# Kernel tuning notes

Hardware: AMD Instinct MI355X
Metric: run time of the kernel (lower is better)

## Reference

```python
import jax, jax.numpy as jnp
import numpy as np

B, S, H = 2, 512, 768
E, M, R, R2 = 64, 64, 128, 128
NER_C, REL_C, SIZE_E, CLS = 10, 8, 32, 101
NEG = -1e30


def _linear(x, w, b):
    # torch nn.Linear convention: w is [out, in]
    return x @ w.T + b


def _span_pool(emb, masks):
    # emb [B,S,H], masks [B,K,S] -> masked max over tokens -> [B,K,H]
    neg = jnp.where(masks[..., None] != 0, 0.0, NEG)  # [B,K,S,1]
    return jnp.max(neg + emb[:, None, :, :], axis=2)


def _classify_spans(input_ids, emb, masks, size_emb, rep_w, rep_b, head_w, head_b):
    pool = _span_pool(emb, masks)                      # [B,K,H]
    cls_idx = jnp.argmax((input_ids == CLS).astype(jnp.int32), axis=1)
    ctx = emb[jnp.arange(emb.shape[0]), cls_idx]       # [B,H] (get_token)
    rep = jnp.concatenate([jnp.broadcast_to(ctx[:, None, :], pool.shape), pool, size_emb], axis=-1)
    clf = _linear(jax.nn.relu(_linear(rep, rep_w, rep_b)), head_w, head_b)
    return clf, pool


def _classify_relations(pool, size_emb, rels, rel_masks, emb, w1, b1, w2, b2, w3, b3):
    Bc = pool.shape[0]
    bidx = jnp.arange(Bc)[:, None, None]
    pairs = pool[bidx, rels].reshape(Bc, rels.shape[1], -1)        # [B,R,2H]
    size_pairs = size_emb[bidx, rels].reshape(Bc, rels.shape[1], -1)  # [B,R,2*SIZE_E]
    # masked max over context tokens (rel mask)
    ctx = jnp.max(jnp.where(rel_masks[..., None] != 0, 0.0, NEG) + emb[:, None, :, :], axis=2)
    ctx = jnp.where(jnp.any(rel_masks != 0, axis=-1)[..., None], ctx, 0.0)
    rel_repr = jnp.concatenate([ctx, pairs, size_pairs], axis=-1)  # [B,R,3H+2*SIZE_E]
    h = jax.nn.relu(_linear(rel_repr, w1, b1))
    h = jax.nn.relu(_linear(h, w2, b2))
    return _linear(h, w3, b3)


def setup_inputs():
    key = jax.random.key(0)
    ks = jax.random.split(key, 24)
    p = lambda k, shape: jax.random.normal(k, shape, jnp.float32) * 0.02
    ids = jax.random.randint(ks[0], (B, S), 2000, 30000)
    ids = ids.at[:, 0].set(CLS)  # exactly one cls token per row
    return dict(
        input_ids=ids,
        entity_masks=jax.random.randint(ks[1], (B, E, S), 0, 2).astype(jnp.int32),
        entity_sizes=jax.random.randint(ks[2], (B, E), 0, 100),
        mention_masks=jax.random.randint(ks[3], (B, M, S), 0, 2).astype(jnp.int32),
        mention_sizes=jax.random.randint(ks[4], (B, M), 0, 100),
        relations=jax.random.randint(ks[5], (B, R, 2), 0, E),
        rel_masks=jax.random.randint(ks[6], (B, R, S), 0, 2).astype(jnp.int32),
        references=jax.random.randint(ks[7], (B, R2, 2), 0, M),
        references_masks=jax.random.randint(ks[8], (B, R2, S), 0, 2).astype(jnp.int32),
        token_embedding=jax.random.normal(ks[9], (B, S, H), jnp.float32),
        ner_size_emb=p(ks[10], (100, SIZE_E)),
        emd_size_emb=p(ks[11], (100, SIZE_E)),
        ner_rep_w=p(ks[12], (H, 2 * H + SIZE_E)), ner_rep_b=jnp.zeros(H, jnp.float32),
        ner_head_w=p(ks[13], (NER_C, H)), ner_head_b=jnp.zeros(NER_C, jnp.float32),
        emd_rep_w=p(ks[14], (H, 2 * H + SIZE_E)), emd_rep_b=jnp.zeros(H, jnp.float32),
        emd_head_w=p(ks[15], (2, H)), emd_head_b=jnp.zeros(2, jnp.float32),
        rel_w1=p(ks[16], (H, 3 * H + 2 * SIZE_E)), rel_b1=jnp.zeros(H, jnp.float32),
        rel_w2=p(ks[17], (H, H)), rel_b2=jnp.zeros(H, jnp.float32),
        rel_w3=p(ks[18], (REL_C, H)), rel_b3=jnp.zeros(REL_C, jnp.float32),
        cr_w1=p(ks[19], (H, 3 * H + 2 * SIZE_E)), cr_b1=jnp.zeros(H, jnp.float32),
        cr_w2=p(ks[20], (H, H)), cr_b2=jnp.zeros(H, jnp.float32),
        cr_w3=p(ks[21], (1, H)), cr_b3=jnp.zeros(1, jnp.float32),
    )


def reference(input_ids, entity_masks, entity_sizes, mention_masks, mention_sizes,
              relations, rel_masks, references, references_masks, token_embedding,
              ner_size_emb, emd_size_emb,
              ner_rep_w, ner_rep_b, ner_head_w, ner_head_b,
              emd_rep_w, emd_rep_b, emd_head_w, emd_head_b,
              rel_w1, rel_b1, rel_w2, rel_b2, rel_w3, rel_b3,
              cr_w1, cr_b1, cr_w2, cr_b2, cr_w3, cr_b3):
    sz = ner_size_emb[entity_sizes]                                    # [B,E,SIZE_E]
    entity_clf, entity_pool = _classify_spans(input_ids, token_embedding, entity_masks, sz,
                                              ner_rep_w, ner_rep_b, ner_head_w, ner_head_b)
    rel_clf = _classify_relations(entity_pool, sz, relations, rel_masks, token_embedding,
                                  rel_w1, rel_b1, rel_w2, rel_b2, rel_w3, rel_b3)
    msz = emd_size_emb[mention_sizes]
    mention_clf, mention_pool = _classify_spans(input_ids, token_embedding, mention_masks, msz,
                                                emd_rep_w, emd_rep_b, emd_head_w, emd_head_b)
    ref_clf = _classify_relations(mention_pool, msz, references, references_masks, token_embedding,
                                  cr_w1, cr_b1, cr_w2, cr_b2, cr_w3, cr_b3)
    return entity_clf, rel_clf, mention_clf, ref_clf
```

## Files before the change

### kernel.cpp

```cpp
#include <hip/hip_runtime.h>
#include <hip/hip_bf16.h>

typedef __hip_bfloat16 bf16;
typedef __attribute__((ext_vector_type(8))) short short8;
typedef __attribute__((ext_vector_type(4))) float f32x4;

#define SS 512
#define HD 768
#define NEGC (-1e30f)

#define WOFF_NER 0
#define WOFF_EMD 1204224
#define WOFF_RW1 2408448
#define WOFF_CW1 4227072
#define WOFF_RW2 6045696
#define WOFF_CW2 6635520
#define W_TOT    7225344
#define CVT_BLOCKS (W_TOT / 4 / 256)

__global__ __launch_bounds__(256) void k_pool_cvt(
    const int* __restrict__ e_masks, const int* __restrict__ m_masks,
    const int* __restrict__ r_masks, const int* __restrict__ c_masks,
    const float* __restrict__ emb, bf16* __restrict__ part, int* __restrict__ flags,
    const float* __restrict__ s0, const float* __restrict__ s1,
    const float* __restrict__ s2, const float* __restrict__ s3,
    const float* __restrict__ s4, const float* __restrict__ s5,
    bf16* __restrict__ wdst)
{
  int bx = blockIdx.x;
  int t  = threadIdx.x;

  if (bx >= 768) {
    size_t i = ((size_t)(bx - 768) * 256 + t) * 4;
    const float* s; size_t off;
    if      (i < WOFF_EMD) { s = s0; off = i; }
    else if (i < WOFF_RW1) { s = s1; off = i - WOFF_EMD; }
    else if (i < WOFF_CW1) { s = s2; off = i - WOFF_RW1; }
    else if (i < WOFF_RW2) { s = s3; off = i - WOFF_CW1; }
    else if (i < WOFF_CW2) { s = s4; off = i - WOFF_RW2; }
    else                   { s = s5; off = i - WOFF_CW2; }
    float4 v = *(const float4*)(s + off);
    wdst[i]     = __hip_bfloat16(v.x);
    wdst[i + 1] = __hip_bfloat16(v.y);
    wdst[i + 2] = __hip_bfloat16(v.z);
    wdst[i + 3] = __hip_bfloat16(v.w);
    return;
  }

  int g  = bx % 48;
  int b  = (bx / 48) & 1;
  int sp = bx / 96;
  int j0 = g * 8;

  const int* marr; int row0;
  if      (j0 < 64)  { marr = e_masks; row0 = b*64  +  j0;        }
  else if (j0 < 128) { marr = m_masks; row0 = b*64  + (j0-64);    }
  else if (j0 < 256) { marr = r_masks; row0 = b*128 + (j0-128);   }
  else               { marr = c_masks; row0 = b*128 + (j0-256);   }

  __shared__ unsigned s_pack[64];
  __shared__ unsigned s_any;
  if (t == 0) s_any = 0u;
  __syncthreads();

  int sbase = sp * 64;
  if (t < 64) {
    unsigned w = 0;
    #pragma unroll
    for (int k = 0; k < 8; k++) {
      int mm = marr[(size_t)(row0 + k) * SS + sbase + t];
      w |= (mm != 0 ? 1u : 0u) << k;
    }
    s_pack[t] = w;
    atomicOr(&s_any, w);
  }
  __syncthreads();

  float acc[8][3];
  #pragma unroll
  for (int k = 0; k < 8; k++)
    #pragma unroll
    for (int i = 0; i < 3; i++) acc[k][i] = -INFINITY;

  const float* ebase = emb + ((size_t)b * SS + sbase) * HD;
  for (int s = 0; s < 64; s++) {
    unsigned wm = s_pack[s];
    const float* ep = ebase + (size_t)s * HD + t;
    float v0 = ep[0];
    float v1 = ep[256];
    float v2 = ep[512];
    #pragma unroll
    for (int k = 0; k < 8; k++) {
      float add = ((wm >> k) & 1u) ? 0.f : NEGC;
      acc[k][0] = fmaxf(acc[k][0], v0 + add);
      acc[k][1] = fmaxf(acc[k][1], v1 + add);
      acc[k][2] = fmaxf(acc[k][2], v2 + add);
    }
  }

  #pragma unroll
  for (int k = 0; k < 8; k++) {
    int sg = b * 384 + j0 + k;
    bf16* dst = part + ((size_t)sp * 768 + sg) * HD;
    dst[t]       = __hip_bfloat16(acc[k][0]);
    dst[t + 256] = __hip_bfloat16(acc[k][1]);
    dst[t + 512] = __hip_bfloat16(acc[k][2]);
  }
  if (t < 8) flags[sp * 768 + b * 384 + j0 + t] = (int)((s_any >> t) & 1u);
}

__global__ __launch_bounds__(256) void k_combine(
    const bf16* __restrict__ part, const int* __restrict__ flags,
    bf16* __restrict__ epool, bf16* __restrict__ mpool,
    bf16* __restrict__ rctx, bf16* __restrict__ cctx)
{
  int sg = blockIdx.x;
  int b = sg / 384, j = sg % 384;
  int any = 0;
  #pragma unroll
  for (int sp = 0; sp < 8; sp++) any |= flags[sp * 768 + sg];
  #pragma unroll
  for (int i = 0; i < 3; i++) {
    int h = threadIdx.x + i * 256;
    float v = -INFINITY;
    #pragma unroll
    for (int sp = 0; sp < 8; sp++)
      v = fmaxf(v, (float)part[((size_t)sp * 768 + sg) * HD + h]);
    if      (j < 64)  epool[((size_t)b*64  + j)       * HD + h] = __hip_bfloat16(v);
    else if (j < 128) mpool[((size_t)b*64  + (j-64))  * HD + h] = __hip_bfloat16(v);
    else if (j < 256) rctx [((size_t)b*128 + (j-128)) * HD + h] = __hip_bfloat16(any ? v : 0.f);
    else              cctx [((size_t)b*128 + (j-256)) * HD + h] = __hip_bfloat16(any ? v : 0.f);
  }
}

__global__ __launch_bounds__(256) void k_rep(
    const int* __restrict__ input_ids, const float* __restrict__ emb,
    const bf16* __restrict__ epool, const bf16* __restrict__ mpool,
    const bf16* __restrict__ rctx, const bf16* __restrict__ cctx,
    const int* __restrict__ esizes, const int* __restrict__ msizes,
    const float* __restrict__ nsemb, const float* __restrict__ esemb,
    const int* __restrict__ relations, const int* __restrict__ references,
    bf16* __restrict__ nrep, bf16* __restrict__ erep,
    bf16* __restrict__ rrep, bf16* __restrict__ crep)
{
  int mode = blockIdx.y;
  if (mode < 2) {
    if (blockIdx.x >= 128) return;
    int which = mode;
    int row = blockIdx.x;
    int b = row >> 6;
    const bf16*  pool  = which ? mpool  : epool;
    const int*   sizes = which ? msizes : esizes;
    const float* st    = which ? esemb  : nsemb;
    bf16* rep = (which ? erep : nrep) + (size_t)row * 1568;

    __shared__ int s_cls;
    if (threadIdx.x == 0) s_cls = SS;
    __syncthreads();
    for (int s = threadIdx.x; s < SS; s += 256)
      if (input_ids[b * SS + s] == 101) atomicMin(&s_cls, s);
    __syncthreads();
    int ci = (s_cls == SS) ? 0 : s_cls;

    const float* ctx = emb + ((size_t)b * SS + ci) * HD;
    const bf16*  pl  = pool + (size_t)row * HD;
    for (int h = threadIdx.x; h < HD; h += 256) {
      rep[h]       = __hip_bfloat16(ctx[h]);
      rep[768 + h] = pl[h];
    }
    if (threadIdx.x < 32)
      rep[1536 + threadIdx.x] = __hip_bfloat16(st[(size_t)sizes[row] * 32 + threadIdx.x]);
  } else {
    int which = mode - 2;
    int row = blockIdx.x;
    int b = row >> 7;
    const int*   rel   = which ? references : relations;
    const bf16*  ctx   = which ? cctx   : rctx;
    const bf16*  pool  = which ? mpool  : epool;
    const int*   sizes = which ? msizes : esizes;
    const float* st    = which ? esemb  : nsemb;
    bf16* rep = (which ? crep : rrep) + (size_t)row * 2368;

    int a0 = rel[row * 2], a1 = rel[row * 2 + 1];
    const bf16* p0 = pool + ((size_t)b * 64 + a0) * HD;
    const bf16* p1 = pool + ((size_t)b * 64 + a1) * HD;
    const bf16* cx = ctx + (size_t)row * HD;
    for (int h = threadIdx.x; h < HD; h += 256) {
      rep[h]        = cx[h];
      rep[768 + h]  = p0[h];
      rep[1536 + h] = p1[h];
    }
    if (threadIdx.x < 32) {
      rep[2304 + threadIdx.x] = __hip_bfloat16(st[(size_t)sizes[b * 64 + a0] * 32 + threadIdx.x]);
      rep[2336 + threadIdx.x] = __hip_bfloat16(st[(size_t)sizes[b * 64 + a1] * 32 + threadIdx.x]);
    }
  }
}

struct GemmArgs  { const void* A; const void* W; const float* bias; void* C; int K; int M; int store_bf16; };
struct GemmArgs4 { GemmArgs p[4]; };

__global__ __launch_bounds__(256) void k_gemm4(GemmArgs4 ga)
{
  GemmArgs g = ga.p[blockIdx.z];
  int mt = blockIdx.x * 32;
  if (mt >= g.M) return;
  int nt = blockIdx.y * 32;

  const short* A = (const short*)g.A;
  const short* W = (const short*)g.W;
  int K_ = g.K;

  int wave = threadIdx.x >> 6, lane = threadIdx.x & 63;
  int lm = lane & 15, quad = lane >> 4;

  const short* a0p = A + (size_t)(mt + lm)      * K_ + quad * 8;
  const short* a1p = A + (size_t)(mt + 16 + lm) * K_ + quad * 8;
  const short* w0p = W + (size_t)(nt + lm)      * K_ + quad * 8;
  const short* w1p = W + (size_t)(nt + 16 + lm) * K_ + quad * 8;

  f32x4 acc00 = {0.f,0.f,0.f,0.f}, acc01 = {0.f,0.f,0.f,0.f};
  f32x4 acc10 = {0.f,0.f,0.f,0.f}, acc11 = {0.f,0.f,0.f,0.f};

  for (int k0 = wave * 32; k0 < K_; k0 += 128) {
    short8 a0 = *(const short8*)(a0p + k0);
    short8 a1 = *(const short8*)(a1p + k0);
    short8 w0 = *(const short8*)(w0p + k0);
    short8 w1 = *(const short8*)(w1p + k0);
    acc00 = __builtin_amdgcn_mfma_f32_16x16x32_bf16(a0, w0, acc00, 0, 0, 0);
    acc01 = __builtin_amdgcn_mfma_f32_16x16x32_bf16(a0, w1, acc01, 0, 0, 0);
    acc10 = __builtin_amdgcn_mfma_f32_16x16x32_bf16(a1, w0, acc10, 0, 0, 0);
    acc11 = __builtin_amdgcn_mfma_f32_16x16x32_bf16(a1, w1, acc11, 0, 0, 0);
  }

  __shared__ float red[4][32][32];
  #pragma unroll
  for (int reg = 0; reg < 4; reg++) {
    int r = quad * 4 + reg;
    red[wave][r][lm]           = acc00[reg];
    red[wave][r][16 + lm]      = acc01[reg];
    red[wave][16 + r][lm]      = acc10[reg];
    red[wave][16 + r][16 + lm] = acc11[reg];
  }
  __syncthreads();

  int c = threadIdx.x & 31;
  int rb = threadIdx.x >> 5;
  float bb = g.bias[nt + c];
  #pragma unroll
  for (int i = 0; i < 4; i++) {
    int r = rb + 8 * i;
    float v = red[0][r][c] + red[1][r][c] + red[2][r][c] + red[3][r][c];
    v = fmaxf(v + bb, 0.f);
    if (g.store_bf16) ((bf16*)g.C)[(size_t)(mt + r) * HD + nt + c] = __hip_bfloat16(v);
    else              ((float*)g.C)[(size_t)(mt + r) * HD + nt + c] = v;
  }
}

__global__ __launch_bounds__(256) void k_heads(
    const float* __restrict__ NH, const float* __restrict__ EH,
    const float* __restrict__ RH2, const float* __restrict__ CH2,
    const float* __restrict__ nhw, const float* __restrict__ nhb,
    const float* __restrict__ ehw, const float* __restrict__ ehb,
    const float* __restrict__ rw3, const float* __restrict__ rb3,
    const float* __restrict__ cw3, const float* __restrict__ cb3,
    float* __restrict__ out)
{
  int gr = blockIdx.x;
  const float* A; const float* W; const float* Bb; float* op; int N;
  if (gr < 128)      { A = NH  + (size_t)gr * HD;        W = nhw; Bb = nhb; N = 10; op = out + (size_t)gr * 10; }
  else if (gr < 384) { int r = gr - 128; A = RH2 + (size_t)r * HD; W = rw3; Bb = rb3; N = 8; op = out + 1280 + (size_t)r * 8; }
  else if (gr < 512) { int r = gr - 384; A = EH  + (size_t)r * HD; W = ehw; Bb = ehb; N = 2; op = out + 3328 + (size_t)r * 2; }
  else               { int r = gr - 512; A = CH2 + (size_t)r * HD; W = cw3; Bb = cb3; N = 1; op = out + 3584 + (size_t)r; }

  float acc[10];
  #pragma unroll
  for (int o = 0; o < 10; o++) acc[o] = 0.f;

  for (int k = threadIdx.x; k < HD; k += 256) {
    float a = A[k];
    #pragma unroll
    for (int o = 0; o < 10; o++) {
      int oo = (o < N) ? o : 0;
      acc[o] += a * W[(size_t)oo * HD + k];
    }
  }

  __shared__ float red[4][10];
  int lane = threadIdx.x & 63, wv = threadIdx.x >> 6;
  #pragma unroll
  for (int o = 0; o < 10; o++) {
    float v = acc[o];
    for (int off = 32; off > 0; off >>= 1) v += __shfl_down(v, off);
    if (lane == 0) red[wv][o] = v;
  }
  __syncthreads();
  if (threadIdx.x < N) {
    float v = red[0][threadIdx.x] + red[1][threadIdx.x] + red[2][threadIdx.x] +
              red[3][threadIdx.x] + Bb[threadIdx.x];
    op[threadIdx.x] = v;
  }
}

extern "C" void kernel_launch(void* const* d_in, const int* in_sizes, int n_in,
                              void* d_out, int out_size, void* d_ws, size_t ws_size,
                              hipStream_t stream)
{
  const int*   input_ids  = (const int*)d_in[0];
  const int*   e_masks    = (const int*)d_in[1];
  const int*   e_sizes    = (const int*)d_in[2];
  const int*   m_masks    = (const int*)d_in[3];
  const int*   m_sizes    = (const int*)d_in[4];
  const int*   relations  = (const int*)d_in[5];
  const int*   r_masks    = (const int*)d_in[6];
  const int*   references = (const int*)d_in[7];
  const int*   c_masks    = (const int*)d_in[8];
  const float* emb        = (const float*)d_in[9];
  const float* nsemb      = (const float*)d_in[10];
  const float* esemb      = (const float*)d_in[11];
  const float* ner_rep_w  = (const float*)d_in[12];
  const float* ner_rep_b  = (const float*)d_in[13];
  const float* ner_head_w = (const float*)d_in[14];
  const float* ner_head_b = (const float*)d_in[15];
  const float* emd_rep_w  = (const float*)d_in[16];
  const float* emd_rep_b  = (const float*)d_in[17];
  const float* emd_head_w = (const float*)d_in[18];
  const float* emd_head_b = (const float*)d_in[19];
  const float* rel_w1 = (const float*)d_in[20];
  const float* rel_b1 = (const float*)d_in[21];
  const float* rel_w2 = (const float*)d_in[22];
  const float* rel_b2 = (const float*)d_in[23];
  const float* rel_w3 = (const float*)d_in[24];
  const float* rel_b3 = (const float*)d_in[25];
  const float* cr_w1 = (const float*)d_in[26];
  const float* cr_b1 = (const float*)d_in[27];
  const float* cr_w2 = (const float*)d_in[28];
  const float* cr_b2 = (const float*)d_in[29];
  const float* cr_w3 = (const float*)d_in[30];
  const float* cr_b3 = (const float*)d_in[31];
  float* out = (float*)d_out;

  float* wsf = (float*)d_ws;
  size_t o = 0;
  int*   FLAGS = (int*)(wsf + o); o += 8 * 768;
  float* NH  = wsf + o; o += (size_t)128 * HD;
  float* EH  = wsf + o; o += (size_t)128 * HD;
  float* RH2 = wsf + o; o += (size_t)256 * HD;
  float* CH2 = wsf + o; o += (size_t)256 * HD;

  bf16* wsb = (bf16*)(wsf + o);
  size_t ob = 0;
  bf16* WBF   = wsb + ob; ob += (size_t)W_TOT;
  bf16* PART  = wsb + ob; ob += (size_t)8 * 768 * HD;
  bf16* EPOOL = wsb + ob; ob += (size_t)128 * HD;
  bf16* MPOOL = wsb + ob; ob += (size_t)128 * HD;
  bf16* RCTX  = wsb + ob; ob += (size_t)256 * HD;
  bf16* CCTX  = wsb + ob; ob += (size_t)256 * HD;
  bf16* NREP  = wsb + ob; ob += (size_t)128 * 1568;
  bf16* EREP  = wsb + ob; ob += (size_t)128 * 1568;
  bf16* RREP  = wsb + ob; ob += (size_t)256 * 2368;
  bf16* CREP  = wsb + ob; ob += (size_t)256 * 2368;
  bf16* RH1   = wsb + ob; ob += (size_t)256 * HD;
  bf16* CH1   = wsb + ob; ob += (size_t)256 * HD;

  k_pool_cvt<<<768 + CVT_BLOCKS, 256, 0, stream>>>(
      e_masks, m_masks, r_masks, c_masks, emb, PART, FLAGS,
      ner_rep_w, emd_rep_w, rel_w1, cr_w1, rel_w2, cr_w2, WBF);
  k_combine<<<768, 256, 0, stream>>>(PART, FLAGS, EPOOL, MPOOL, RCTX, CCTX);
  k_rep<<<dim3(256, 4), 256, 0, stream>>>(input_ids, emb, EPOOL, MPOOL, RCTX, CCTX,
                                          e_sizes, m_sizes, nsemb, esemb,
                                          relations, references,
                                          NREP, EREP, RREP, CREP);
  {
    GemmArgs4 ga;
    ga.p[0] = { NREP, WBF + WOFF_NER, ner_rep_b, NH,  1568, 128, 0 };
    ga.p[1] = { EREP, WBF + WOFF_EMD, emd_rep_b, EH,  1568, 128, 0 };
    ga.p[2] = { RREP, WBF + WOFF_RW1, rel_b1,    RH1, 2368, 256, 1 };
    ga.p[3] = { CREP, WBF + WOFF_CW1, cr_b1,     CH1, 2368, 256, 1 };
    k_gemm4<<<dim3(8, 24, 4), 256, 0, stream>>>(ga);
  }
  {
    GemmArgs4 ga;
    ga.p[0] = { RH1, WBF + WOFF_RW2, rel_b2, RH2, 768, 256, 0 };
    ga.p[1] = { CH1, WBF + WOFF_CW2, cr_b2,  CH2, 768, 256, 0 };
    ga.p[2] = ga.p[0]; ga.p[3] = ga.p[1];
    k_gemm4<<<dim3(8, 24, 2), 256, 0, stream>>>(ga);
  }
  k_heads<<<768, 256, 0, stream>>>(NH, EH, RH2, CH2,
                                   ner_head_w, ner_head_b, emd_head_w, emd_head_b,
                                   rel_w3, rel_b3, cr_w3, cr_b3, out);
}
```

Before: 209.2 us.

## Fuse pooling, rep gather and head projections; drop combine/rep/heads kernels

The pooling kernel now scans all 512 tokens per block split across hidden-dim chunks, so the partial-max buffer and the combine kernel go away. The weight conversion becomes a grid-stride loop spread over the same blocks. Size embeddings, the CLS context and zeroing of the output are also produced in this kernel. The first GEMM gathers its A operand directly from the pooled/context buffers instead of a materialized concatenated rep. The final small head projections are fused into the GEMM epilogues via atomicAdd into the zeroed output. This cuts the launch count from six kernels to three and removes the intermediate traffic, at the cost of atomics, a longer serial token loop per block, and indirect A loads.

```diff
diff --git a/kernel.cpp b/kernel.cpp
--- a/kernel.cpp
+++ b/kernel.cpp
@@ -16,22 +16,32 @@
 #define WOFF_RW2 6045696
 #define WOFF_CW2 6635520
 #define W_TOT    7225344
-#define CVT_BLOCKS (W_TOT / 4 / 256)
+#define PC_BLOCKS 576
+#define CVT_UNITS (W_TOT / 1024)
 
 __global__ __launch_bounds__(256) void k_pool_cvt(
     const int* __restrict__ e_masks, const int* __restrict__ m_masks,
     const int* __restrict__ r_masks, const int* __restrict__ c_masks,
-    const float* __restrict__ emb, bf16* __restrict__ part, int* __restrict__ flags,
+    const float* __restrict__ emb, const int* __restrict__ input_ids,
+    const int* __restrict__ esizes, const int* __restrict__ msizes,
+    const float* __restrict__ nsemb, const float* __restrict__ esemb,
     const float* __restrict__ s0, const float* __restrict__ s1,
     const float* __restrict__ s2, const float* __restrict__ s3,
     const float* __restrict__ s4, const float* __restrict__ s5,
-    bf16* __restrict__ wdst)
+    bf16* __restrict__ wdst,
+    bf16* __restrict__ epool, bf16* __restrict__ mpool,
+    bf16* __restrict__ rctx, bf16* __restrict__ cctx,
+    bf16* __restrict__ sze, bf16* __restrict__ szm,
+    bf16* __restrict__ ctxb, float* __restrict__ out)
 {
-  int bx = blockIdx.x;
   int t  = threadIdx.x;
-
-  if (bx >= 768) {
-    size_t i = ((size_t)(bx - 768) * 256 + t) * 4;
+  int g  = blockIdx.x;
+  int b  = blockIdx.y;
+  int hc = blockIdx.z;
+
+  int bx = g + 48 * b + 96 * hc;
+  for (int u = bx; u < CVT_UNITS; u += PC_BLOCKS) {
+    size_t i = ((size_t)u * 256 + t) * 4;
     const float* s; size_t off;
     if      (i < WOFF_EMD) { s = s0; off = i; }
     else if (i < WOFF_RW1) { s = s1; off = i - WOFF_EMD; }
@@ -44,203 +54,157 @@
     wdst[i + 1] = __hip_bfloat16(v.y);
     wdst[i + 2] = __hip_bfloat16(v.z);
     wdst[i + 3] = __hip_bfloat16(v.w);
-    return;
-  }
-
-  int g  = bx % 48;
-  int b  = (bx / 48) & 1;
-  int sp = bx / 96;
+  }
+
   int j0 = g * 8;
-
   const int* marr; int row0;
   if      (j0 < 64)  { marr = e_masks; row0 = b*64  +  j0;        }
   else if (j0 < 128) { marr = m_masks; row0 = b*64  + (j0-64);    }
   else if (j0 < 256) { marr = r_masks; row0 = b*128 + (j0-128);   }
   else               { marr = c_masks; row0 = b*128 + (j0-256);   }
 
-  __shared__ unsigned s_pack[64];
+  __shared__ unsigned s_pack[SS];
   __shared__ unsigned s_any;
-  if (t == 0) s_any = 0u;
-  __syncthreads();
-
-  int sbase = sp * 64;
-  if (t < 64) {
+  __shared__ int s_cls;
+  if (t == 0) { s_any = 0u; s_cls = SS; }
+  __syncthreads();
+
+  unsigned wor = 0;
+  for (int s = t; s < SS; s += 256) {
     unsigned w = 0;
     #pragma unroll
     for (int k = 0; k < 8; k++) {
-      int mm = marr[(size_t)(row0 + k) * SS + sbase + t];
+      int mm = marr[(size_t)(row0 + k) * SS + s];
       w |= (mm != 0 ? 1u : 0u) << k;
     }
-    s_pack[t] = w;
-    atomicOr(&s_any, w);
-  }
-  __syncthreads();
-
-  float acc[8][3];
-  #pragma unroll
-  for (int k = 0; k < 8; k++)
-    #pragma unroll
-    for (int i = 0; i < 3; i++) acc[k][i] = -INFINITY;
-
-  const float* ebase = emb + ((size_t)b * SS + sbase) * HD;
-  for (int s = 0; s < 64; s++) {
-    unsigned wm = s_pack[s];
-    const float* ep = ebase + (size_t)s * HD + t;
-    float v0 = ep[0];
-    float v1 = ep[256];
-    float v2 = ep[512];
-    #pragma unroll
-    for (int k = 0; k < 8; k++) {
-      float add = ((wm >> k) & 1u) ? 0.f : NEGC;
-      acc[k][0] = fmaxf(acc[k][0], v0 + add);
-      acc[k][1] = fmaxf(acc[k][1], v1 + add);
-      acc[k][2] = fmaxf(acc[k][2], v2 + add);
-    }
-  }
-
-  #pragma unroll
-  for (int k = 0; k < 8; k++) {
-    int sg = b * 384 + j0 + k;
-    bf16* dst = part + ((size_t)sp * 768 + sg) * HD;
-    dst[t]       = __hip_bfloat16(acc[k][0]);
-    dst[t + 256] = __hip_bfloat16(acc[k][1]);
-    dst[t + 512] = __hip_bfloat16(acc[k][2]);
-  }
-  if (t < 8) flags[sp * 768 + b * 384 + j0 + t] = (int)((s_any >> t) & 1u);
-}
-
-__global__ __launch_bounds__(256) void k_combine(
-    const bf16* __restrict__ part, const int* __restrict__ flags,
-    bf16* __restrict__ epool, bf16* __restrict__ mpool,
-    bf16* __restrict__ rctx, bf16* __restrict__ cctx)
-{
-  int sg = blockIdx.x;
-  int b = sg / 384, j = sg % 384;
-  int any = 0;
-  #pragma unroll
-  for (int sp = 0; sp < 8; sp++) any |= flags[sp * 768 + sg];
-  #pragma unroll
-  for (int i = 0; i < 3; i++) {
-    int h = threadIdx.x + i * 256;
-    float v = -INFINITY;
-    #pragma unroll
-    for (int sp = 0; sp < 8; sp++)
-      v = fmaxf(v, (float)part[((size_t)sp * 768 + sg) * HD + h]);
+    s_pack[s] = w;
+    wor |= w;
+  }
+  atomicOr(&s_any, wor);
+  __syncthreads();
+
+  int hl = t & 127, sh = t >> 7;
+  int h = hc * 128 + hl;
+  const float* ep = emb + (size_t)b * SS * HD + h;
+  float a0 = -INFINITY, a1 = -INFINITY, a2 = -INFINITY, a3 = -INFINITY;
+  #pragma unroll 4
+  for (int s = 0; s < SS; s++) {
+    float v = ep[(size_t)s * HD];
+    unsigned wm = s_pack[s] >> (sh * 4);
+    a0 = (wm & 1u) ? fmaxf(a0, v) : a0;
+    a1 = (wm & 2u) ? fmaxf(a1, v) : a1;
+    a2 = (wm & 4u) ? fmaxf(a2, v) : a2;
+    a3 = (wm & 8u) ? fmaxf(a3, v) : a3;
+  }
+
+  unsigned anyw = s_any;
+  float acc[4] = { a0, a1, a2, a3 };
+  #pragma unroll
+  for (int kk = 0; kk < 4; kk++) {
+    int kbit = sh * 4 + kk;
+    int j = j0 + kbit;
+    float v = acc[kk];
+    int any = (anyw >> kbit) & 1u;
     if      (j < 64)  epool[((size_t)b*64  + j)       * HD + h] = __hip_bfloat16(v);
     else if (j < 128) mpool[((size_t)b*64  + (j-64))  * HD + h] = __hip_bfloat16(v);
     else if (j < 256) rctx [((size_t)b*128 + (j-128)) * HD + h] = __hip_bfloat16(any ? v : 0.f);
     else              cctx [((size_t)b*128 + (j-256)) * HD + h] = __hip_bfloat16(any ? v : 0.f);
   }
+
+  if (hc == 5) {
+    if (g == 0) {
+      for (int i = t; i < 64 * 32; i += 256) {
+        int r = b * 64 + (i >> 5), c = i & 31;
+        sze[(size_t)r * 32 + c] = __hip_bfloat16(nsemb[(size_t)esizes[r] * 32 + c]);
+      }
+    } else if (g == 1) {
+      for (int i = t; i < 64 * 32; i += 256) {
+        int r = b * 64 + (i >> 5), c = i & 31;
+        szm[(size_t)r * 32 + c] = __hip_bfloat16(esemb[(size_t)msizes[r] * 32 + c]);
+      }
+    } else if (g == 2) {
+      for (int s = t; s < SS; s += 256)
+        if (input_ids[b * SS + s] == 101) atomicMin(&s_cls, s);
+      __syncthreads();
+      int ci = (s_cls == SS) ? 0 : s_cls;
+      for (int hh = t; hh < HD; hh += 256)
+        ctxb[(size_t)b * HD + hh] = __hip_bfloat16(emb[((size_t)b * SS + ci) * HD + hh]);
+    } else if (g == 3) {
+      for (int i = t; i < 1920; i += 256) out[b * 1920 + i] = 0.f;
+    }
+  }
 }
 
-__global__ __launch_bounds__(256) void k_rep(
-    const int* __restrict__ input_ids, const float* __restrict__ emb,
-    const bf16* __restrict__ epool, const bf16* __restrict__ mpool,
-    const bf16* __restrict__ rctx, const bf16* __restrict__ cctx,
-    const int* __restrict__ esizes, const int* __restrict__ msizes,
-    const float* __restrict__ nsemb, const float* __restrict__ esemb,
-    const int* __restrict__ relations, const int* __restrict__ references,
-    bf16* __restrict__ nrep, bf16* __restrict__ erep,
-    bf16* __restrict__ rrep, bf16* __restrict__ crep)
+struct P1 {
+  const bf16 *ctx, *pool, *sz; const int* ridx;
+  const short* W; const float* bias;
+  bf16* C;
+  const float *hw, *hb; float* outp;
+  int is_rel, N, K, Mtiles;
+};
+struct P1x4 { P1 p[4]; };
+
+__global__ __launch_bounds__(256, 2) void k_gemm1(P1x4 args)
 {
-  int mode = blockIdx.y;
-  if (mode < 2) {
-    if (blockIdx.x >= 128) return;
-    int which = mode;
-    int row = blockIdx.x;
-    int b = row >> 6;
-    const bf16*  pool  = which ? mpool  : epool;
-    const int*   sizes = which ? msizes : esizes;
-    const float* st    = which ? esemb  : nsemb;
-    bf16* rep = (which ? erep : nrep) + (size_t)row * 1568;
-
-    __shared__ int s_cls;
-    if (threadIdx.x == 0) s_cls = SS;
-    __syncthreads();
-    for (int s = threadIdx.x; s < SS; s += 256)
-      if (input_ids[b * SS + s] == 101) atomicMin(&s_cls, s);
-    __syncthreads();
-    int ci = (s_cls == SS) ? 0 : s_cls;
-
-    const float* ctx = emb + ((size_t)b * SS + ci) * HD;
-    const bf16*  pl  = pool + (size_t)row * HD;
-    for (int h = threadIdx.x; h < HD; h += 256) {
-      rep[h]       = __hip_bfloat16(ctx[h]);
-      rep[768 + h] = pl[h];
-    }
-    if (threadIdx.x < 32)
-      rep[1536 + threadIdx.x] = __hip_bfloat16(st[(size_t)sizes[row] * 32 + threadIdx.x]);
-  } else {
-    int which = mode - 2;
-    int row = blockIdx.x;
-    int b = row >> 7;
-    const int*   rel   = which ? references : relations;
-    const bf16*  ctx   = which ? cctx   : rctx;
-    const bf16*  pool  = which ? mpool  : epool;
-    const int*   sizes = which ? msizes : esizes;
-    const float* st    = which ? esemb  : nsemb;
-    bf16* rep = (which ? crep : rrep) + (size_t)row * 2368;
-
-    int a0 = rel[row * 2], a1 = rel[row * 2 + 1];
-    const bf16* p0 = pool + ((size_t)b * 64 + a0) * HD;
-    const bf16* p1 = pool + ((size_t)b * 64 + a1) * HD;
-    const bf16* cx = ctx + (size_t)row * HD;
-    for (int h = threadIdx.x; h < HD; h += 256) {
-      rep[h]        = cx[h];
-      rep[768 + h]  = p0[h];
-      rep[1536 + h] = p1[h];
-    }
-    if (threadIdx.x < 32) {
-      rep[2304 + threadIdx.x] = __hip_bfloat16(st[(size_t)sizes[b * 64 + a0] * 32 + threadIdx.x]);
-      rep[2336 + threadIdx.x] = __hip_bfloat16(st[(size_t)sizes[b * 64 + a1] * 32 + threadIdx.x]);
-    }
-  }
-}
-
-struct GemmArgs  { const void* A; const void* W; const float* bias; void* C; int K; int M; int store_bf16; };
-struct GemmArgs4 { GemmArgs p[4]; };
-
-__global__ __launch_bounds__(256) void k_gemm4(GemmArgs4 ga)
-{
-  GemmArgs g = ga.p[blockIdx.z];
-  int mt = blockIdx.x * 32;
-  if (mt >= g.M) return;
-  int nt = blockIdx.y * 32;
-
-  const short* A = (const short*)g.A;
-  const short* W = (const short*)g.W;
-  int K_ = g.K;
-
+  P1 g = args.p[blockIdx.z];
+  int x = blockIdx.x;
+  if (x >= g.Mtiles) return;
+  int mt = x * 32, nt = blockIdx.y * 32;
   int wave = threadIdx.x >> 6, lane = threadIdx.x & 63;
   int lm = lane & 15, quad = lane >> 4;
-
-  const short* a0p = A + (size_t)(mt + lm)      * K_ + quad * 8;
-  const short* a1p = A + (size_t)(mt + 16 + lm) * K_ + quad * 8;
-  const short* w0p = W + (size_t)(nt + lm)      * K_ + quad * 8;
-  const short* w1p = W + (size_t)(nt + 16 + lm) * K_ + quad * 8;
+  int K_ = g.K;
+
+  const bf16 *g0[2], *g1[2], *g2[2], *g3[2], *g4[2];
+  int rr[2] = { mt + lm, mt + 16 + lm };
+  #pragma unroll
+  for (int i = 0; i < 2; i++) {
+    int r = rr[i];
+    if (g.is_rel) {
+      int b = r >> 7;
+      int i0 = g.ridx[2 * r], i1 = g.ridx[2 * r + 1];
+      g0[i] = g.ctx  + (size_t)r * HD;
+      g1[i] = g.pool + (size_t)(b * 64 + i0) * HD;
+      g2[i] = g.pool + (size_t)(b * 64 + i1) * HD;
+      g3[i] = g.sz   + (size_t)(b * 64 + i0) * 32;
+      g4[i] = g.sz   + (size_t)(b * 64 + i1) * 32;
+    } else {
+      g0[i] = g.ctx  + (size_t)(r >> 6) * HD;
+      g1[i] = g.pool + (size_t)r * HD;
+      g2[i] = g.sz   + (size_t)r * 32;
+      g3[i] = g2[i]; g4[i] = g2[i];
+    }
+  }
+  const short* w0p = g.W + (size_t)(nt + lm)      * K_ + quad * 8;
+  const short* w1p = g.W + (size_t)(nt + 16 + lm) * K_ + quad * 8;
 
   f32x4 acc00 = {0.f,0.f,0.f,0.f}, acc01 = {0.f,0.f,0.f,0.f};
   f32x4 acc10 = {0.f,0.f,0.f,0.f}, acc11 = {0.f,0.f,0.f,0.f};
 
-  for (int k0 = wave * 32; k0 < K_; k0 += 128) {
-    short8 a0 = *(const short8*)(a0p + k0);
-    short8 a1 = *(const short8*)(a1p + k0);
-    short8 w0 = *(const short8*)(w0p + k0);
-    short8 w1 = *(const short8*)(w1p + k0);
+  for (int k32 = wave * 32; k32 < K_; k32 += 128) {
+    const bf16 *b0, *b1;
+    if      (k32 < 768)  { b0 = g0[0] + k32;          b1 = g0[1] + k32;          }
+    else if (k32 < 1536) { b0 = g1[0] + (k32 - 768);  b1 = g1[1] + (k32 - 768);  }
+    else if (k32 < 2304) { b0 = g2[0] + (k32 - 1536); b1 = g2[1] + (k32 - 1536); }
+    else if (k32 < 2336) { b0 = g3[0] + (k32 - 2304); b1 = g3[1] + (k32 - 2304); }
+    else                 { b0 = g4[0] + (k32 - 2336); b1 = g4[1] + (k32 - 2336); }
+    short8 a0 = *(const short8*)((const short*)b0 + quad * 8);
+    short8 a1 = *(const short8*)((const short*)b1 + quad * 8);
+    short8 w0 = *(const short8*)(w0p + k32);
+    short8 w1 = *(const short8*)(w1p + k32);
     acc00 = __builtin_amdgcn_mfma_f32_16x16x32_bf16(a0, w0, acc00, 0, 0, 0);
     acc01 = __builtin_amdgcn_mfma_f32_16x16x32_bf16(a0, w1, acc01, 0, 0, 0);
     acc10 = __builtin_amdgcn_mfma_f32_16x16x32_bf16(a1, w0, acc10, 0, 0, 0);
     acc11 = __builtin_amdgcn_mfma_f32_16x16x32_bf16(a1, w1, acc11, 0, 0, 0);
   }
 
-  __shared__ float red[4][32][32];
+  __shared__ float smem[4 * 32 * 32];
   #pragma unroll
   for (int reg = 0; reg < 4; reg++) {
     int r = quad * 4 + reg;
-    red[wave][r][lm]           = acc00[reg];
-    red[wave][r][16 + lm]      = acc01[reg];
-    red[wave][16 + r][lm]      = acc10[reg];
-    red[wave][16 + r][16 + lm] = acc11[reg];
+    smem[wave*1024 + r*32 + lm]             = acc00[reg];
+    smem[wave*1024 + r*32 + 16 + lm]        = acc01[reg];
+    smem[wave*1024 + (16 + r)*32 + lm]      = acc10[reg];
+    smem[wave*1024 + (16 + r)*32 + 16 + lm] = acc11[reg];
   }
   __syncthreads();
 
@@ -250,55 +214,90 @@
   #pragma unroll
   for (int i = 0; i < 4; i++) {
     int r = rb + 8 * i;
-    float v = red[0][r][c] + red[1][r][c] + red[2][r][c] + red[3][r][c];
+    float v = smem[r*32 + c] + smem[1024 + r*32 + c] + smem[2048 + r*32 + c] + smem[3072 + r*32 + c];
     v = fmaxf(v + bb, 0.f);
-    if (g.store_bf16) ((bf16*)g.C)[(size_t)(mt + r) * HD + nt + c] = __hip_bfloat16(v);
-    else              ((float*)g.C)[(size_t)(mt + r) * HD + nt + c] = v;
+    if (g.C) g.C[(size_t)(mt + r) * HD + nt + c] = __hip_bfloat16(v);
+    else     smem[r*32 + c] = v;
+  }
+  __syncthreads();
+
+  if (!g.C) {
+    int r = threadIdx.x >> 3, oi = threadIdx.x & 7;
+    for (int o = oi; o < g.N; o += 8) {
+      float s = 0.f;
+      #pragma unroll
+      for (int cc = 0; cc < 32; cc++) {
+        int c2 = (cc + r) & 31;
+        s += smem[r*32 + c2] * g.hw[(size_t)o * HD + nt + c2];
+      }
+      if (blockIdx.y == 0) s += g.hb[o];
+      atomicAdd(g.outp + (size_t)(mt + r) * g.N + o, s);
+    }
   }
 }
 
-__global__ __launch_bounds__(256) void k_heads(
-    const float* __restrict__ NH, const float* __restrict__ EH,
-    const float* __restrict__ RH2, const float* __restrict__ CH2,
-    const float* __restrict__ nhw, const float* __restrict__ nhb,
-    const float* __restrict__ ehw, const float* __restrict__ ehb,
-    const float* __restrict__ rw3, const float* __restrict__ rb3,
-    const float* __restrict__ cw3, const float* __restrict__ cb3,
-    float* __restrict__ out)
+struct P2 { const short* A; const short* W; const float* bias;
+            const float *hw, *hb; float* outp; int N; };
+struct P2x2 { P2 p[2]; };
+
+__global__ __launch_bounds__(256, 2) void k_gemm2(P2x2 args)
 {
-  int gr = blockIdx.x;
-  const float* A; const float* W; const float* Bb; float* op; int N;
-  if (gr < 128)      { A = NH  + (size_t)gr * HD;        W = nhw; Bb = nhb; N = 10; op = out + (size_t)gr * 10; }
-  else if (gr < 384) { int r = gr - 128; A = RH2 + (size_t)r * HD; W = rw3; Bb = rb3; N = 8; op = out + 1280 + (size_t)r * 8; }
-  else if (gr < 512) { int r = gr - 384; A = EH  + (size_t)r * HD; W = ehw; Bb = ehb; N = 2; op = out + 3328 + (size_t)r * 2; }
-  else               { int r = gr - 512; A = CH2 + (size_t)r * HD; W = cw3; Bb = cb3; N = 1; op = out + 3584 + (size_t)r; }
-
-  float acc[10];
-  #pragma unroll
-  for (int o = 0; o < 10; o++) acc[o] = 0.f;
-
-  for (int k = threadIdx.x; k < HD; k += 256) {
-    float a = A[k];
+  P2 g = args.p[blockIdx.z];
+  int mt = blockIdx.x * 32, nt = blockIdx.y * 32;
+  int wave = threadIdx.x >> 6, lane = threadIdx.x & 63;
+  int lm = lane & 15, quad = lane >> 4;
+
+  const short* a0p = g.A + (size_t)(mt + lm)      * HD + quad * 8;
+  const short* a1p = g.A + (size_t)(mt + 16 + lm) * HD + quad * 8;
+  const short* w0p = g.W + (size_t)(nt + lm)      * HD + quad * 8;
+  const short* w1p = g.W + (size_t)(nt + 16 + lm) * HD + quad * 8;
+
+  f32x4 acc00 = {0.f,0.f,0.f,0.f}, acc01 = {0.f,0.f,0.f,0.f};
+  f32x4 acc10 = {0.f,0.f,0.f,0.f}, acc11 = {0.f,0.f,0.f,0.f};
+
+  for (int k32 = wave * 32; k32 < HD; k32 += 128) {
+    short8 a0 = *(const short8*)(a0p + k32);
+    short8 a1 = *(const short8*)(a1p + k32);
+    short8 w0 = *(const short8*)(w0p + k32);
+    short8 w1 = *(const short8*)(w1p + k32);
+    acc00 = __builtin_amdgcn_mfma_f32_16x16x32_bf16(a0, w0, acc00, 0, 0, 0);
+    acc01 = __builtin_amdgcn_mfma_f32_16x16x32_bf16(a0, w1, acc01, 0, 0, 0);
+    acc10 = __builtin_amdgcn_mfma_f32_16x16x32_bf16(a1, w0, acc10, 0, 0, 0);
+    acc11 = __builtin_amdgcn_mfma_f32_16x16x32_bf16(a1, w1, acc11, 0, 0, 0);
+  }
+
+  __shared__ float smem[4 * 32 * 32];
+  #pragma unroll
+  for (int reg = 0; reg < 4; reg++) {
+    int r = quad * 4 + reg;
+    smem[wave*1024 + r*32 + lm]             = acc00[reg];
+    smem[wave*1024 + r*32 + 16 + lm]        = acc01[reg];
+    smem[wave*1024 + (16 + r)*32 + lm]      = acc10[reg];
+    smem[wave*1024 + (16 + r)*32 + 16 + lm] = acc11[reg];
+  }
+  __syncthreads();
+
+  int c = threadIdx.x & 31;
+  int rb = threadIdx.x >> 5;
+  float bb = g.bias[nt + c];
+  #pragma unroll
+  for (int i = 0; i < 4; i++) {
+    int r = rb + 8 * i;
+    float v = smem[r*32 + c] + smem[1024 + r*32 + c] + smem[2048 + r*32 + c] + smem[3072 + r*32 + c];
+    smem[r*32 + c] = fmaxf(v + bb, 0.f);
+  }
+  __syncthreads();
+
+  int r = threadIdx.x >> 3, oi = threadIdx.x & 7;
+  for (int o = oi; o < g.N; o += 8) {
+    float s = 0.f;
     #pragma unroll
-    for (int o = 0; o < 10; o++) {
-      int oo = (o < N) ? o : 0;
-      acc[o] += a * W[(size_t)oo * HD + k];
-    }
-  }
-
-  __shared__ float red[4][10];
-  int lane = threadIdx.x & 63, wv = threadIdx.x >> 6;
-  #pragma unroll
-  for (int o = 0; o < 10; o++) {
-    float v = acc[o];
-    for (int off = 32; off > 0; off >>= 1) v += __shfl_down(v, off);
-    if (lane == 0) red[wv][o] = v;
-  }
-  __syncthreads();
-  if (threadIdx.x < N) {
-    float v = red[0][threadIdx.x] + red[1][threadIdx.x] + red[2][threadIdx.x] +
-              red[3][threadIdx.x] + Bb[threadIdx.x];
-    op[threadIdx.x] = v;
+    for (int cc = 0; cc < 32; cc++) {
+      int c2 = (cc + r) & 31;
+      s += smem[r*32 + c2] * g.hw[(size_t)o * HD + nt + c2];
+    }
+    if (blockIdx.y == 0) s += g.hb[o];
+    atomicAdd(g.outp + (size_t)(mt + r) * g.N + o, s);
   }
 }
 
@@ -340,53 +339,40 @@
   const float* cr_b3 = (const float*)d_in[31];
   float* out = (float*)d_out;
 
-  float* wsf = (float*)d_ws;
-  size_t o = 0;
-  int*   FLAGS = (int*)(wsf + o); o += 8 * 768;
-  float* NH  = wsf + o; o += (size_t)128 * HD;
-  float* EH  = wsf + o; o += (size_t)128 * HD;
-  float* RH2 = wsf + o; o += (size_t)256 * HD;
-  float* CH2 = wsf + o; o += (size_t)256 * HD;
-
-  bf16* wsb = (bf16*)(wsf + o);
+  bf16* wsb = (bf16*)d_ws;
   size_t ob = 0;
   bf16* WBF   = wsb + ob; ob += (size_t)W_TOT;
-  bf16* PART  = wsb + ob; ob += (size_t)8 * 768 * HD;
   bf16* EPOOL = wsb + ob; ob += (size_t)128 * HD;
   bf16* MPOOL = wsb + ob; ob += (size_t)128 * HD;
   bf16* RCTX  = wsb + ob; ob += (size_t)256 * HD;
   bf16* CCTX  = wsb + ob; ob += (size_t)256 * HD;
-  bf16* NREP  = wsb + ob; ob += (size_t)128 * 1568;
-  bf16* EREP  = wsb + ob; ob += (size_t)128 * 1568;
-  bf16* RREP  = wsb + ob; ob += (size_t)256 * 2368;
-  bf16* CREP  = wsb + ob; ob += (size_t)256 * 2368;
+  bf16* SZE   = wsb + ob; ob += (size_t)128 * 32;
+  bf16* SZM   = wsb + ob; ob += (size_t)128 * 32;
+  bf16* CTXB  = wsb + ob; ob += (size_t)2 * HD;
   bf16* RH1   = wsb + ob; ob += (size_t)256 * HD;
   bf16* CH1   = wsb + ob; ob += (size_t)256 * HD;
 
-  k_pool_cvt<<<768 + CVT_BLOCKS, 256, 0, stream>>>(
-      e_masks, m_masks, r_masks, c_masks, emb, PART, FLAGS,
-      ner_rep_w, emd_rep_w, rel_w1, cr_w1, rel_w2, cr_w2, WBF);
-  k_combine<<<768, 256, 0, stream>>>(PART, FLAGS, EPOOL, MPOOL, RCTX, CCTX);
-  k_rep<<<dim3(256, 4), 256, 0, stream>>>(input_ids, emb, EPOOL, MPOOL, RCTX, CCTX,
-                                          e_sizes, m_sizes, nsemb, esemb,
-                                          relations, references,
-                                          NREP, EREP, RREP, CREP);
-  {
-    GemmArgs4 ga;
-    ga.p[0] = { NREP, WBF + WOFF_NER, ner_rep_b, NH,  1568, 128, 0 };
-    ga.p[1] = { EREP, WBF + WOFF_EMD, emd_rep_b, EH,  1568, 128, 0 };
-    ga.p[2] = { RREP, WBF + WOFF_RW1, rel_b1,    RH1, 2368, 256, 1 };
-    ga.p[3] = { CREP, WBF + WOFF_CW1, cr_b1,     CH1, 2368, 256, 1 };
-    k_gemm4<<<dim3(8, 24, 4), 256, 0, stream>>>(ga);
-  }
-  {
-    GemmArgs4 ga;
-    ga.p[0] = { RH1, WBF + WOFF_RW2, rel_b2, RH2, 768, 256, 0 };
-    ga.p[1] = { CH1, WBF + WOFF_CW2, cr_b2,  CH2, 768, 256, 0 };
-    ga.p[2] = ga.p[0]; ga.p[3] = ga.p[1];
-    k_gemm4<<<dim3(8, 24, 2), 256, 0, stream>>>(ga);
-  }
-  k_heads<<<768, 256, 0, stream>>>(NH, EH, RH2, CH2,
-                                   ner_head_w, ner_head_b, emd_head_w, emd_head_b,
-                                   rel_w3, rel_b3, cr_w3, cr_b3, out);
+  k_pool_cvt<<<dim3(48, 2, 6), 256, 0, stream>>>(
+      e_masks, m_masks, r_masks, c_masks, emb, input_ids,
+      e_sizes, m_sizes, nsemb, esemb,
+      ner_rep_w, emd_rep_w, rel_w1, cr_w1, rel_w2, cr_w2, WBF,
+      EPOOL, MPOOL, RCTX, CCTX, SZE, SZM, CTXB, out);
+
+  P1x4 a1;
+  a1.p[0] = { CTXB, EPOOL, SZE, nullptr,    (const short*)(WBF + WOFF_NER), ner_rep_b,
+              nullptr, ner_head_w, ner_head_b, out,        0, 10, 1568, 4 };
+  a1.p[1] = { CTXB, MPOOL, SZM, nullptr,    (const short*)(WBF + WOFF_EMD), emd_rep_b,
+              nullptr, emd_head_w, emd_head_b, out + 3328, 0, 2,  1568, 4 };
+  a1.p[2] = { RCTX, EPOOL, SZE, relations,  (const short*)(WBF + WOFF_RW1), rel_b1,
+              RH1, nullptr, nullptr, nullptr,              1, 0,  2368, 8 };
+  a1.p[3] = { CCTX, MPOOL, SZM, references, (const short*)(WBF + WOFF_CW1), cr_b1,
+              CH1, nullptr, nullptr, nullptr,              1, 0,  2368, 8 };
+  k_gemm1<<<dim3(8, 24, 4), 256, 0, stream>>>(a1);
+
+  P2x2 a2;
+  a2.p[0] = { (const short*)RH1, (const short*)(WBF + WOFF_RW2), rel_b2,
+              rel_w3, rel_b3, out + 1280, 8 };
+  a2.p[1] = { (const short*)CH1, (const short*)(WBF + WOFF_CW2), cr_b2,
+              cr_w3, cr_b3, out + 3584, 1 };
+  k_gemm2<<<dim3(8, 24, 2), 256, 0, stream>>>(a2);
 }
```

New measurement: 254.4 us. 1.22x slower.
